# Kernel tuning notes

Hardware: AMD Instinct MI355X
Metric: run time of the kernel (lower is better)

## Reference

```python
import jax, jax.numpy as jnp
import numpy as np

EPS = 1e-5
NEG_INF = -1e38


def q_shift(x, H, W, gamma=0.25, s=1):
    # x: (B, T, C) with T = H*W. Four channel groups shifted by 1 pixel in +W,-W,+H,-H.
    B, T, C = x.shape
    g = int(C * gamma)
    x4 = x.reshape(B, H, W, C)
    o0 = jnp.pad(x4[..., 0:g], ((0, 0), (0, 0), (s, 0), (0, 0)))[:, :, :W, :]      # shift right along W
    o1 = jnp.pad(x4[..., g:2 * g], ((0, 0), (0, 0), (0, s), (0, 0)))[:, :, s:, :]  # shift left along W
    o2 = jnp.pad(x4[..., 2 * g:3 * g], ((0, 0), (s, 0), (0, 0), (0, 0)))[:, :H, :, :]  # shift down along H
    o3 = jnp.pad(x4[..., 3 * g:4 * g], ((0, 0), (0, s), (0, 0), (0, 0)))[:, s:, :, :]  # shift up along H
    parts = [o0, o1, o2, o3]
    if 4 * g < C:
        parts.append(jnp.zeros((B, H, W, C - 4 * g), x.dtype))
    return jnp.concatenate(parts, axis=-1).reshape(B, T, C)


def wkv(w, u, k, v):
    # Numerically-stable RWKV WKV recurrence.
    # w,u: (C,); k,v: (B,T,C) -> y: (B,T,C)
    B, T, C = k.shape

    def step(carry, kv):
        a, b, p = carry
        kt, vt = kv
        ww = u + kt
        p2 = jnp.maximum(p, ww)
        e1 = jnp.exp(p - p2)
        e2 = jnp.exp(ww - p2)
        y = (e1 * a + e2 * vt) / (e1 * b + e2)
        ww2 = p + w
        p3 = jnp.maximum(ww2, kt)
        f1 = jnp.exp(ww2 - p3)
        f2 = jnp.exp(kt - p3)
        return (f1 * a + f2 * vt, f1 * b + f2, p3), y

    init = (jnp.zeros((B, C), k.dtype), jnp.zeros((B, C), k.dtype),
            jnp.full((B, C), NEG_INF, k.dtype))
    kT = jnp.swapaxes(k, 0, 1)
    vT = jnp.swapaxes(v, 0, 1)
    _, ys = jax.lax.scan(step, init, (kT, vT))
    return jnp.swapaxes(ys, 0, 1)


def layer_norm(x, g, b):
    m = jnp.mean(x, axis=-1, keepdims=True)
    v = jnp.mean(jnp.square(x - m), axis=-1, keepdims=True)
    return (x - m) * jax.lax.rsqrt(v + EPS) * g + b


def setup_inputs() -> dict:
    key = jax.random.key(0)
    ks = jax.random.split(key, 16)
    B, H, W, C = 8, 64, 64, 768
    T = H * W
    sc = 1.0 / np.sqrt(C)
    inp = {
        "x": jax.random.normal(ks[0], (B, T, C), jnp.float32),
        "spatial_decay": jax.random.normal(ks[1], (C,), jnp.float32) * 0.1,
        "spatial_first": jax.random.normal(ks[2], (C,), jnp.float32) * 0.1,
        "mix_k": jax.random.uniform(ks[3], (1, 1, C), jnp.float32),
        "mix_v": jax.random.uniform(ks[4], (1, 1, C), jnp.float32),
        "mix_r": jax.random.uniform(ks[5], (1, 1, C), jnp.float32),
        "Wk": jax.random.normal(ks[6], (C, C), jnp.float32) * sc,
        "Wv": jax.random.normal(ks[7], (C, C), jnp.float32) * sc,
        "Wr": jax.random.normal(ks[8], (C, C), jnp.float32) * sc,
        "Wo": jax.random.normal(ks[9], (C, C), jnp.float32) * sc,
        "ln_g": jnp.ones((C,), jnp.float32),
        "ln_b": jnp.zeros((C,), jnp.float32),
        "Wd1": jax.random.normal(ks[10], (C, C // 4), jnp.float32) * sc,
        "bd1": jnp.zeros((C // 4,), jnp.float32),
        "Wd2": jax.random.normal(ks[11], (C // 4, C), jnp.float32) * (2.0 / np.sqrt(C)),
        "bd2": jnp.full((C,), -3.0, jnp.float32),
        "H": H,
        "W": W,
    }
    return inp


def reference(x, spatial_decay, spatial_first, mix_k, mix_v, mix_r,
              Wk, Wv, Wr, Wo, ln_g, ln_b, Wd1, bd1, Wd2, bd2, H, W):
    B, T, C = x.shape
    xx = q_shift(x, H, W)
    xk = x * mix_k + xx * (1.0 - mix_k)
    xv = x * mix_v + xx * (1.0 - mix_v)
    xr = x * mix_r + xx * (1.0 - mix_r)
    k = xk @ Wk
    v = xv @ Wv
    sr = jax.nn.sigmoid(xr @ Wr)
    # frequency-adaptive decay modulation from global context
    gctx = jnp.mean(x, axis=1)                       # (B, C)
    h = jnp.tanh(gctx @ Wd1 + bd1)                   # (B, C/4)
    mod = jax.nn.sigmoid(h @ Wd2 + bd2)              # (B, C)
    w = spatial_decay + jnp.mean(mod, axis=0)        # (C,)
    y = wkv(w, spatial_first, k, v)                  # (B, T, C)
    y = layer_norm(y, ln_g, ln_b)
    return (sr * y) @ Wo
```

## Files before the change

kernel.cpp:

```cpp
#include <hip/hip_runtime.h>
#include <hip/hip_bf16.h>

typedef __hip_bfloat16 bf16;
typedef short short8 __attribute__((ext_vector_type(8)));
typedef float f32x4 __attribute__((ext_vector_type(4)));

#define T_SEQ 4096
#define HH 64
#define WW2 64
#define C_DIM 768
#define CQ 192
#define LCH 32
#define NCH (T_SEQ / LCH)
#define NCG (C_DIM / 8)

__device__ __forceinline__ float b2f(bf16 h) { return __bfloat162float(h); }
__device__ __forceinline__ bf16 f2b(float f) { return __float2bfloat16(f); }
__device__ __forceinline__ float sigmoid_stable(float m) {
  float e = __expf(-fabsf(m));
  return (m >= 0.f) ? 1.f / (1.f + e) : e / (1.f + e);
}

union V16 { uint4 u; bf16 h[8]; };

__global__ void k_detect(const unsigned* __restrict__ p, int* __restrict__ flag) {
  if (threadIdx.x == 0 && blockIdx.x == 0)
    *flag = ((p[0] & 0xFFFFu) == 0u) ? 1 : 0;
}

__global__ void k_convert_b(const void* __restrict__ src, bf16* __restrict__ dst,
                            int n, const int* __restrict__ flag) {
  int i = blockIdx.x * blockDim.x + threadIdx.x;
  if (i >= n) return;
  dst[i] = (*flag) ? f2b(((const float*)src)[i]) : ((const bf16*)src)[i];
}

__global__ void k_convert_f(const void* __restrict__ src, float* __restrict__ dst,
                            int n, const int* __restrict__ flag) {
  int i = blockIdx.x * blockDim.x + threadIdx.x;
  if (i >= n) return;
  dst[i] = (*flag) ? ((const float*)src)[i] : b2f(((const bf16*)src)[i]);
}

__global__ void k_transpose_d(const void* __restrict__ src, bf16* __restrict__ dst,
                              const int* __restrict__ flag) {
  __shared__ bf16 tile[32][33];
  bool f32 = (*flag != 0);
  int bx = blockIdx.x * 32, by = blockIdx.y * 32;
  int tx = threadIdx.x, ty = threadIdx.y;
  for (int j = ty; j < 32; j += 8) {
    size_t idx = (size_t)(by + j) * C_DIM + bx + tx;
    tile[j][tx] = f32 ? f2b(((const float*)src)[idx]) : ((const bf16*)src)[idx];
  }
  __syncthreads();
  for (int j = ty; j < 32; j += 8)
    dst[(size_t)(bx + j) * C_DIM + by + tx] = tile[tx][j];
}

__global__ void k_shift_mix1(const void* __restrict__ xsrc,
                             const float* __restrict__ mix,
                             bf16* __restrict__ dst, int BT,
                             const int* __restrict__ flag) {
  int idx = blockIdx.x * blockDim.x + threadIdx.x;
  if (idx >= BT * (C_DIM / 8)) return;
  bool f32 = (*flag != 0);
  int c8 = (idx % (C_DIM / 8)) * 8;
  int tg = idx / (C_DIM / 8);
  int t = tg & (T_SEQ - 1);
  int hh = t >> 6, ww = t & (WW2 - 1);
  int g = c8 / CQ;
  int d; bool valid;
  if (g == 0)      { valid = (ww >= 1);        d = -1;   }
  else if (g == 1) { valid = (ww <= WW2 - 2);  d = 1;    }
  else if (g == 2) { valid = (hh >= 1);        d = -WW2; }
  else             { valid = (hh <= HH - 2);   d = WW2;  }
  ptrdiff_t base = (ptrdiff_t)tg * C_DIM + c8;
  float fx[8], fxx[8];
  if (f32) {
    const float* xp = (const float*)xsrc;
#pragma unroll
    for (int i = 0; i < 8; i++) fx[i] = xp[base + i];
    if (valid) {
#pragma unroll
      for (int i = 0; i < 8; i++) fxx[i] = xp[base + (ptrdiff_t)d * C_DIM + i];
    } else {
#pragma unroll
      for (int i = 0; i < 8; i++) fxx[i] = 0.f;
    }
  } else {
    const bf16* xp = (const bf16*)xsrc;
    V16 xin; xin.u = *(const uint4*)(xp + base);
    V16 xxv;
    if (valid) xxv.u = *(const uint4*)(xp + base + (ptrdiff_t)d * C_DIM);
    else       xxv.u = make_uint4(0u, 0u, 0u, 0u);
#pragma unroll
    for (int i = 0; i < 8; i++) { fx[i] = b2f(xin.h[i]); fxx[i] = b2f(xxv.h[i]); }
  }
  V16 o;
#pragma unroll
  for (int i = 0; i < 8; i++)
    o.h[i] = f2b(fxx[i] + mix[c8 + i] * (fx[i] - fxx[i]));
  *(uint4*)(dst + base) = o.u;
}

__global__ void k_gctx(const void* __restrict__ xsrc, float* __restrict__ gctx,
                       const int* __restrict__ flag) {
  bool f32 = (*flag != 0);
  int c = threadIdx.x;
  int chunk = blockIdx.x;
  int b = blockIdx.y;
  size_t base = ((size_t)b * T_SEQ + (size_t)chunk * 128) * C_DIM + c;
  float s = 0.f;
  if (f32) {
    const float* p = (const float*)xsrc;
    for (int t = 0; t < 128; t++) s += p[base + (size_t)t * C_DIM];
  } else {
    const bf16* p = (const bf16*)xsrc;
    for (int t = 0; t < 128; t++) s += b2f(p[base + (size_t)t * C_DIM]);
  }
  atomicAdd(&gctx[b * C_DIM + c], s);
}

__global__ void k_mod(const float* __restrict__ gctx,
                      const bf16* __restrict__ Wd1, const float* __restrict__ bd1,
                      const bf16* __restrict__ Wd2, const float* __restrict__ bd2,
                      float* __restrict__ wsum, int B) {
  __shared__ float hsh[CQ];
  int b = blockIdx.x, j = threadIdx.x;
  const float invT = 1.0f / (float)T_SEQ;
  float acc = bd1[j];
  for (int i = 0; i < C_DIM; i++)
    acc += (gctx[b * C_DIM + i] * invT) * b2f(Wd1[(size_t)i * CQ + j]);
  hsh[j] = tanhf(acc);
  __syncthreads();
  float invB = 1.0f / (float)B;
  for (int cc = j; cc < C_DIM; cc += CQ) {
    float m = bd2[cc];
    for (int jj = 0; jj < CQ; jj++)
      m += hsh[jj] * b2f(Wd2[(size_t)jj * C_DIM + cc]);
    atomicAdd(&wsum[cc], sigmoid_stable(m) * invB);
  }
}

__device__ __forceinline__ void g2l16(const void* g, void* s) {
  __builtin_amdgcn_global_load_lds(
      (const __attribute__((address_space(1))) unsigned int*)g,
      (__attribute__((address_space(3))) unsigned int*)s, 16, 0, 0);
}

template <int MODE>
__global__ __launch_bounds__(256) void k_gemm_bt(const bf16* __restrict__ A,
                                                 const bf16* __restrict__ Bt,
                                                 void* __restrict__ Cout,
                                                 const int* __restrict__ flag) {
  const int K = C_DIM, N = C_DIM;
  __shared__ bf16 sA[128 * 32];
  __shared__ bf16 sB[128 * 32];
  int tid = threadIdx.x;
  int wv = tid >> 6, lane = tid & 63;
  int lm = lane & 15, quad = lane >> 4;
  int m0 = blockIdx.x * 128, n0 = blockIdx.y * 128;
  int wm = (wv & 1) * 64, wn = (wv >> 1) * 64;
  bool f32out = (MODE == 2) && (*flag != 0);

  f32x4 acc[4][4];
#pragma unroll
  for (int i = 0; i < 4; i++)
#pragma unroll
    for (int j = 0; j < 4; j++) acc[i][j] = f32x4{0.f, 0.f, 0.f, 0.f};

  const bf16* Abase = A + (size_t)m0 * K;
  const bf16* Bbase = Bt + (size_t)n0 * K;
  int ci0 = wv * 128 + lane;
  int ci1 = wv * 128 + 64 + lane;

  for (int kc = 0; kc < K; kc += 32) {
    g2l16(Abase + (size_t)(ci0 >> 2) * K + kc + (ci0 & 3) * 8, (char*)sA + (size_t)(wv * 128) * 16);
    g2l16(Abase + (size_t)(ci1 >> 2) * K + kc + (ci1 & 3) * 8, (char*)sA + (size_t)(wv * 128 + 64) * 16);
    g2l16(Bbase + (size_t)(ci0 >> 2) * K + kc + (ci0 & 3) * 8, (char*)sB + (size_t)(wv * 128) * 16);
    g2l16(Bbase + (size_t)(ci1 >> 2) * K + kc + (ci1 & 3) * 8, (char*)sB + (size_t)(wv * 128 + 64) * 16);
    __syncthreads();
    short8 af[4], bfr[4];
#pragma unroll
    for (int i = 0; i < 4; i++)
      af[i] = *(const short8*)(sA + (size_t)(wm + i * 16 + lm) * 32 + quad * 8);
#pragma unroll
    for (int j = 0; j < 4; j++)
      bfr[j] = *(const short8*)(sB + (size_t)(wn + j * 16 + lm) * 32 + quad * 8);
#pragma unroll
    for (int i = 0; i < 4; i++)
#pragma unroll
      for (int j = 0; j < 4; j++)
        acc[i][j] = __builtin_amdgcn_mfma_f32_16x16x32_bf16(af[i], bfr[j], acc[i][j], 0, 0, 0);
    __syncthreads();
  }
#pragma unroll
  for (int i = 0; i < 4; i++)
#pragma unroll
    for (int j = 0; j < 4; j++)
#pragma unroll
      for (int r = 0; r < 4; r++) {
        int m = wm + i * 16 + quad * 4 + r;
        int n = wn + j * 16 + lm;
        float v = acc[i][j][r];
        if (MODE == 1) v = sigmoid_stable(v);
        size_t oidx = (size_t)(m0 + m) * N + n0 + n;
        if (MODE == 2) {
          if (f32out) ((float*)Cout)[oidx] = v;
          else        ((bf16*)Cout)[oidx] = f2b(v);
        } else {
          ((bf16*)Cout)[oidx] = f2b(v);
        }
      }
}


__global__ __launch_bounds__(256) void k_wkv_p1(
    const bf16* __restrict__ kb, const bf16* __restrict__ vb,
    const float* __restrict__ sd, const float* __restrict__ wsum,
    float* __restrict__ ca, float* __restrict__ cb, float* __restrict__ cp, int B) {
  int gid = blockIdx.x * 256 + threadIdx.x;
  if (gid >= B * NCH * NCG) return;
  int cg = gid % NCG;
  int ch = (gid / NCG) % NCH;
  int b  = gid / (NCG * NCH);
  int c0 = cg * 8;
  float w[8], a[8], bb[8], p[8];
#pragma unroll
  for (int i = 0; i < 8; i++) {
    w[i] = sd[c0 + i] + wsum[c0 + i];
    a[i] = 0.f; bb[i] = 0.f; p[i] = -1e38f;
  }
  const bf16* kp = kb + ((size_t)b * T_SEQ + (size_t)ch * LCH) * C_DIM + c0;
  const bf16* vp = vb + ((size_t)b * T_SEQ + (size_t)ch * LCH) * C_DIM + c0;
  V16 kv, vv, kn, vn;
  kv.u = *(const uint4*)kp;
  vv.u = *(const uint4*)vp;
  kn = kv; vn = vv;
  for (int t = 0; t < LCH; t++) {
    if (t + 1 < LCH) {
      kn.u = *(const uint4*)(kp + (size_t)(t + 1) * C_DIM);
      vn.u = *(const uint4*)(vp + (size_t)(t + 1) * C_DIM);
    }
#pragma unroll
    for (int i = 0; i < 8; i++) {
      float kt = b2f(kv.h[i]), vt = b2f(vv.h[i]);
      float ww2 = p[i] + w[i];
      float p3 = fmaxf(ww2, kt);
      float f1 = __expf(ww2 - p3);
      float f2 = __expf(kt - p3);
      a[i] = f1 * a[i] + f2 * vt;
      bb[i] = f1 * bb[i] + f2;
      p[i] = p3;
    }
    kv = kn; vv = vn;
  }
  size_t so = ((size_t)b * NCH + ch) * C_DIM + c0;
#pragma unroll
  for (int i = 0; i < 8; i++) { ca[so + i] = a[i]; cb[so + i] = bb[i]; cp[so + i] = p[i]; }
}

__global__ void k_wkv_p2(float* __restrict__ ca, float* __restrict__ cb,
                         float* __restrict__ cp,
                         const float* __restrict__ sd, const float* __restrict__ wsum,
                         int B) {
  int tid = blockIdx.x * blockDim.x + threadIdx.x;
  if (tid >= B * C_DIM) return;
  int b = tid / C_DIM, c = tid % C_DIM;
  float wL = (sd[c] + wsum[c]) * (float)LCH;
  float a = 0.f, bb = 0.f, p = -1e38f;
  for (int base = 0; base < NCH; base += 16) {
    float la[16], lb[16], lp[16];
#pragma unroll
    for (int j = 0; j < 16; j++) {
      size_t idx = ((size_t)b * NCH + base + j) * C_DIM + c;
      la[j] = ca[idx]; lb[j] = cb[idx]; lp[j] = cp[idx];
    }
#pragma unroll
    for (int j = 0; j < 16; j++) {
      size_t idx = ((size_t)b * NCH + base + j) * C_DIM + c;
      ca[idx] = a; cb[idx] = bb; cp[idx] = p;
      float pw = p + wL;
      float pn = fmaxf(pw, lp[j]);
      float e1 = __expf(pw - pn);
      float e2 = __expf(lp[j] - pn);
      a = e1 * a + e2 * la[j];
      bb = e1 * bb + e2 * lb[j];
      p = pn;
    }
  }
}

__global__ __launch_bounds__(256) void k_wkv_p3(
    const bf16* __restrict__ kb, const bf16* __restrict__ vb,
    const float* __restrict__ sd, const float* __restrict__ sf,
    const float* __restrict__ wsum,
    const float* __restrict__ ca, const float* __restrict__ cb,
    const float* __restrict__ cp, bf16* __restrict__ y, int B) {
  int gid = blockIdx.x * 256 + threadIdx.x;
  if (gid >= B * NCH * NCG) return;
  int cg = gid % NCG;
  int ch = (gid / NCG) % NCH;
  int b  = gid / (NCG * NCH);
  int c0 = cg * 8;
  size_t so = ((size_t)b * NCH + ch) * C_DIM + c0;
  float w[8], u[8], aa[8], bb[8], pp[8];
#pragma unroll
  for (int i = 0; i < 8; i++) {
    w[i] = sd[c0 + i] + wsum[c0 + i];
    u[i] = sf[c0 + i];
    aa[i] = ca[so + i]; bb[i] = cb[so + i]; pp[i] = cp[so + i];
  }
  const bf16* kp = kb + ((size_t)b * T_SEQ + (size_t)ch * LCH) * C_DIM + c0;
  const bf16* vp = vb + ((size_t)b * T_SEQ + (size_t)ch * LCH) * C_DIM + c0;
  bf16* yp = y + ((size_t)b * T_SEQ + (size_t)ch * LCH) * C_DIM + c0;
  V16 kv, vv, kn, vn;
  kv.u = *(const uint4*)kp;
  vv.u = *(const uint4*)vp;
  kn = kv; vn = vv;
  for (int t = 0; t < LCH; t++) {
    if (t + 1 < LCH) {
      kn.u = *(const uint4*)(kp + (size_t)(t + 1) * C_DIM);
      vn.u = *(const uint4*)(vp + (size_t)(t + 1) * C_DIM);
    }
    V16 o;
#pragma unroll
    for (int i = 0; i < 8; i++) {
      float kt = b2f(kv.h[i]), vt = b2f(vv.h[i]);
      float ww = u[i] + kt;
      float p2 = fmaxf(pp[i], ww);
      float e1 = __expf(pp[i] - p2);
      float e2 = __expf(ww - p2);
      o.h[i] = f2b((e1 * aa[i] + e2 * vt) / (e1 * bb[i] + e2));
      float ww2 = pp[i] + w[i];
      float p3 = fmaxf(ww2, kt);
      float f1 = __expf(ww2 - p3);
      float f2 = __expf(kt - p3);
      aa[i] = f1 * aa[i] + f2 * vt;
      bb[i] = f1 * bb[i] + f2;
      pp[i] = p3;
    }
    *(uint4*)(yp + (size_t)t * C_DIM) = o.u;
    kv = kn; vv = vn;
  }
}

__global__ __launch_bounds__(256) void k_ln_mul(const bf16* __restrict__ y,
                                                const bf16* __restrict__ sr,
                                                const float* __restrict__ lng,
                                                const float* __restrict__ lnb,
                                                bf16* __restrict__ out) {
  int row = blockIdx.x;
  int tid = threadIdx.x;
  const bf16* yr = y + (size_t)row * C_DIM;
  float v0 = b2f(yr[tid]), v1 = b2f(yr[tid + 256]), v2 = b2f(yr[tid + 512]);
  float s1 = v0 + v1 + v2;
  float s2 = v0 * v0 + v1 * v1 + v2 * v2;
#pragma unroll
  for (int off = 32; off >= 1; off >>= 1) {
    s1 += __shfl_xor(s1, off, 64);
    s2 += __shfl_xor(s2, off, 64);
  }
  __shared__ float sh1[4], sh2[4];
  int wv = tid >> 6, lane = tid & 63;
  if (lane == 0) { sh1[wv] = s1; sh2[wv] = s2; }
  __syncthreads();
  float t1 = sh1[0] + sh1[1] + sh1[2] + sh1[3];
  float t2 = sh2[0] + sh2[1] + sh2[2] + sh2[3];
  float mean = t1 * (1.f / (float)C_DIM);
  float var = t2 * (1.f / (float)C_DIM) - mean * mean;
  float rstd = rsqrtf(var + 1e-5f);
  const bf16* srr = sr + (size_t)row * C_DIM;
  bf16* orow = out + (size_t)row * C_DIM;
  float vv[3] = {v0, v1, v2};
#pragma unroll
  for (int kk = 0; kk < 3; kk++) {
    int c = tid + kk * 256;
    float r = (vv[kk] - mean) * rstd * lng[c] + lnb[c];
    orow[c] = f2b(r * b2f(srr[c]));
  }
}

extern "C" void kernel_launch(void* const* d_in, const int* in_sizes, int n_in,
                              void* d_out, int out_size, void* d_ws, size_t ws_size,
                              hipStream_t stream) {
  const void* x   = d_in[0];
  const void* sd  = d_in[1];
  const void* sf  = d_in[2];
  const void* mk  = d_in[3];
  const void* mv  = d_in[4];
  const void* mr  = d_in[5];
  const void* Wk  = d_in[6];
  const void* Wv  = d_in[7];
  const void* Wr  = d_in[8];
  const void* Wo  = d_in[9];
  const void* lng = d_in[10];
  const void* lnb = d_in[11];
  const void* Wd1 = d_in[12];
  const void* bd1 = d_in[13];
  const void* Wd2 = d_in[14];
  const void* bd2 = d_in[15];

  const int C = in_sizes[1];
  const int BT = in_sizes[0] / C;
  const int B = BT / T_SEQ;

  char* ws = (char*)d_ws;
  const size_t S = (size_t)BT * C * sizeof(bf16);
  const size_t WB = (size_t)C * C * sizeof(bf16);
  const size_t WD = (size_t)C * CQ * sizeof(bf16);
  bf16* slot0 = (bf16*)(ws + 0 * S);
  bf16* slot1 = (bf16*)(ws + 1 * S);
  char* p = ws + 2 * S;
  bf16* WkT = (bf16*)p; p += WB;
  bf16* WvT = (bf16*)p; p += WB;
  bf16* WrT = (bf16*)p; p += WB;
  bf16* WoT = (bf16*)p; p += WB;
  bf16* Wd1c = (bf16*)p; p += WD;
  bf16* Wd2c = (bf16*)p; p += WD;
  float* sd_f  = (float*)p; p += C * 4;
  float* sf_f  = (float*)p; p += C * 4;
  float* mk_f  = (float*)p; p += C * 4;
  float* mv_f  = (float*)p; p += C * 4;
  float* mr_f  = (float*)p; p += C * 4;
  float* lng_f = (float*)p; p += C * 4;
  float* lnb_f = (float*)p; p += C * 4;
  float* bd2_f = (float*)p; p += C * 4;
  float* bd1_f = (float*)p; p += CQ * 4;
  float* gctx  = (float*)p; p += (size_t)B * C * 4;
  float* wsum  = (float*)p; p += C * 4;
  int* flag    = (int*)p; p += 16;
  p = (char*)(((uintptr_t)p + 15) & ~(uintptr_t)15);
  float* ca = (float*)p; p += (size_t)B * NCH * C * 4;
  float* cb = (float*)p; p += (size_t)B * NCH * C * 4;
  float* cp = (float*)p; p += (size_t)B * NCH * C * 4;

  bf16* stage = (bf16*)d_out;

  k_detect<<<1, 64, 0, stream>>>((const unsigned*)lng, flag);
  hipMemsetAsync(gctx, 0, (size_t)(B * C + C) * sizeof(float), stream);

  k_convert_f<<<3, 256, 0, stream>>>(sd,  sd_f,  C, flag);
  k_convert_f<<<3, 256, 0, stream>>>(sf,  sf_f,  C, flag);
  k_convert_f<<<3, 256, 0, stream>>>(mk,  mk_f,  C, flag);
  k_convert_f<<<3, 256, 0, stream>>>(mv,  mv_f,  C, flag);
  k_convert_f<<<3, 256, 0, stream>>>(mr,  mr_f,  C, flag);
  k_convert_f<<<3, 256, 0, stream>>>(lng, lng_f, C, flag);
  k_convert_f<<<3, 256, 0, stream>>>(lnb, lnb_f, C, flag);
  k_convert_f<<<3, 256, 0, stream>>>(bd2, bd2_f, C, flag);
  k_convert_f<<<1, 256, 0, stream>>>(bd1, bd1_f, CQ, flag);
  k_convert_b<<<(C * CQ + 255) / 256, 256, 0, stream>>>(Wd1, Wd1c, C * CQ, flag);
  k_convert_b<<<(C * CQ + 255) / 256, 256, 0, stream>>>(Wd2, Wd2c, C * CQ, flag);

  dim3 tb(32, 8), tg(C / 32, C / 32);
  k_transpose_d<<<tg, tb, 0, stream>>>(Wk, WkT, flag);
  k_transpose_d<<<tg, tb, 0, stream>>>(Wv, WvT, flag);
  k_transpose_d<<<tg, tb, 0, stream>>>(Wr, WrT, flag);
  k_transpose_d<<<tg, tb, 0, stream>>>(Wo, WoT, flag);

  k_gctx<<<dim3(32, B), C, 0, stream>>>(x, gctx, flag);
  k_mod<<<B, CQ, 0, stream>>>(gctx, Wd1c, bd1_f, Wd2c, bd2_f, wsum, B);

  int nthr = BT * (C / 8);
  int nblk = (nthr + 255) / 256;
  dim3 gg(BT / 128, C / 128);

  k_shift_mix1<<<nblk, 256, 0, stream>>>(x, mk_f, stage, BT, flag);
  k_gemm_bt<0><<<gg, 256, 0, stream>>>(stage, WkT, slot0, flag);
  k_shift_mix1<<<nblk, 256, 0, stream>>>(x, mv_f, stage, BT, flag);
  k_gemm_bt<0><<<gg, 256, 0, stream>>>(stage, WvT, slot1, flag);

  int scan_threads = B * NCH * NCG;
  k_wkv_p1<<<(scan_threads + 255) / 256, 256, 0, stream>>>(slot0, slot1, sd_f, wsum, ca, cb, cp, B);
  k_wkv_p2<<<(B * C + 255) / 256, 256, 0, stream>>>(ca, cb, cp, sd_f, wsum, B);
  k_wkv_p3<<<(scan_threads + 255) / 256, 256, 0, stream>>>(slot0, slot1, sd_f, sf_f, wsum, ca, cb, cp, stage, B);

  k_shift_mix1<<<nblk, 256, 0, stream>>>(x, mr_f, slot0, BT, flag);
  k_gemm_bt<1><<<gg, 256, 0, stream>>>(slot0, WrT, slot1, flag);
  k_ln_mul<<<BT, 256, 0, stream>>>(stage, slot1, lng_f, lnb_f, slot0);
  k_gemm_bt<2><<<gg, 256, 0, stream>>>(slot0, WoT, d_out, flag);
}
```

Baseline: 716.2 us.

## Fuse prep kernels, merge k/v shift-mix, stage GEMM epilogue through LDS

Replaces the many tiny conversion/transpose launches and the flag-detect kernel with one prep kernel, one batched transpose kernel, and inline dtype detection. The k and v shift-mix passes are merged so x is read once for both. The GEMM epilogue now goes through shared memory so each row is written with wide vector stores, and the grid is reordered so N varies fastest. LayerNorm is vectorized with 192 threads handling 4 elements each. These target launch overhead, redundant reads of x, and scattered scalar stores, at the cost of extra LDS syncs in the epilogue.

```diff
diff --git a/kernel.cpp b/kernel.cpp
--- a/kernel.cpp
+++ b/kernel.cpp
@@ -20,32 +20,58 @@
   float e = __expf(-fabsf(m));
   return (m >= 0.f) ? 1.f / (1.f + e) : e / (1.f + e);
 }
+__device__ __forceinline__ bool is_f32(const void* lng) {
+  return ((const unsigned*)lng)[0] % 65536u == 0u;
+}
 
 union V16 { uint4 u; bf16 h[8]; };
-
-__global__ void k_detect(const unsigned* __restrict__ p, int* __restrict__ flag) {
-  if (threadIdx.x == 0 && blockIdx.x == 0)
-    *flag = ((p[0] & 0xFFFFu) == 0u) ? 1 : 0;
-}
-
-__global__ void k_convert_b(const void* __restrict__ src, bf16* __restrict__ dst,
-                            int n, const int* __restrict__ flag) {
-  int i = blockIdx.x * blockDim.x + threadIdx.x;
-  if (i >= n) return;
-  dst[i] = (*flag) ? f2b(((const float*)src)[i]) : ((const bf16*)src)[i];
-}
-
-__global__ void k_convert_f(const void* __restrict__ src, float* __restrict__ dst,
-                            int n, const int* __restrict__ flag) {
-  int i = blockIdx.x * blockDim.x + threadIdx.x;
-  if (i >= n) return;
-  dst[i] = (*flag) ? ((const float*)src)[i] : b2f(((const bf16*)src)[i]);
-}
-
-__global__ void k_transpose_d(const void* __restrict__ src, bf16* __restrict__ dst,
-                              const int* __restrict__ flag) {
+union V8f { float4 f; float x[4]; };
+
+__global__ void k_prep(const void* sd, const void* sf, const void* mk, const void* mv,
+                       const void* mr, const void* lng, const void* lnb, const void* bd2,
+                       const void* bd1, const void* Wd1, const void* Wd2,
+                       float* sd_f, float* sf_f, float* mk_f, float* mv_f, float* mr_f,
+                       float* lng_f, float* lnb_f, float* bd2_f, float* bd1_f,
+                       bf16* Wd1c, bf16* Wd2c) {
+  bool f32 = is_f32(lng);
+  int i = blockIdx.x * 256 + threadIdx.x;
+  if (i < 6144) {
+    int a = i / 768, idx = i % 768;
+    const void* s; float* d;
+    switch (a) {
+      case 0: s = sd;  d = sd_f;  break;
+      case 1: s = sf;  d = sf_f;  break;
+      case 2: s = mk;  d = mk_f;  break;
+      case 3: s = mv;  d = mv_f;  break;
+      case 4: s = mr;  d = mr_f;  break;
+      case 5: s = lng; d = lng_f; break;
+      case 6: s = lnb; d = lnb_f; break;
+      default: s = bd2; d = bd2_f; break;
+    }
+    d[idx] = f32 ? ((const float*)s)[idx] : b2f(((const bf16*)s)[idx]);
+  } else if (i < 6336) {
+    int idx = i - 6144;
+    bd1_f[idx] = f32 ? ((const float*)bd1)[idx] : b2f(((const bf16*)bd1)[idx]);
+  } else if (i < 6336 + 147456) {
+    int idx = i - 6336;
+    Wd1c[idx] = f32 ? f2b(((const float*)Wd1)[idx]) : ((const bf16*)Wd1)[idx];
+  } else if (i < 6336 + 294912) {
+    int idx = i - 153792;
+    Wd2c[idx] = f32 ? f2b(((const float*)Wd2)[idx]) : ((const bf16*)Wd2)[idx];
+  }
+}
+
+__global__ void k_transpose4(const void* W0, const void* W1, const void* W2, const void* W3,
+                             bf16* D0, bf16* D1, bf16* D2, bf16* D3, const void* lng) {
   __shared__ bf16 tile[32][33];
-  bool f32 = (*flag != 0);
+  bool f32 = is_f32(lng);
+  const void* src; bf16* dst;
+  switch (blockIdx.z) {
+    case 0: src = W0; dst = D0; break;
+    case 1: src = W1; dst = D1; break;
+    case 2: src = W2; dst = D2; break;
+    default: src = W3; dst = D3; break;
+  }
   int bx = blockIdx.x * 32, by = blockIdx.y * 32;
   int tx = threadIdx.x, ty = threadIdx.y;
   for (int j = ty; j < 32; j += 8) {
@@ -57,23 +83,27 @@
     dst[(size_t)(bx + j) * C_DIM + by + tx] = tile[tx][j];
 }
 
-__global__ void k_shift_mix1(const void* __restrict__ xsrc,
-                             const float* __restrict__ mix,
-                             bf16* __restrict__ dst, int BT,
-                             const int* __restrict__ flag) {
-  int idx = blockIdx.x * blockDim.x + threadIdx.x;
-  if (idx >= BT * (C_DIM / 8)) return;
-  bool f32 = (*flag != 0);
-  int c8 = (idx % (C_DIM / 8)) * 8;
-  int tg = idx / (C_DIM / 8);
-  int t = tg & (T_SEQ - 1);
+__device__ __forceinline__ void shift_geom(int t, int c8, int& d, bool& valid) {
   int hh = t >> 6, ww = t & (WW2 - 1);
   int g = c8 / CQ;
-  int d; bool valid;
   if (g == 0)      { valid = (ww >= 1);        d = -1;   }
   else if (g == 1) { valid = (ww <= WW2 - 2);  d = 1;    }
   else if (g == 2) { valid = (hh >= 1);        d = -WW2; }
   else             { valid = (hh <= HH - 2);   d = WW2;  }
+}
+
+__global__ void k_shift_mix2(const void* __restrict__ xsrc,
+                             const float* __restrict__ mka, const float* __restrict__ mva,
+                             bf16* __restrict__ dk, bf16* __restrict__ dv,
+                             int BT, const void* lng) {
+  int idx = blockIdx.x * blockDim.x + threadIdx.x;
+  if (idx >= BT * (C_DIM / 8)) return;
+  bool f32 = is_f32(lng);
+  int c8 = (idx % (C_DIM / 8)) * 8;
+  int tg = idx / (C_DIM / 8);
+  int t = tg & (T_SEQ - 1);
+  int d; bool valid;
+  shift_geom(t, c8, d, valid);
   ptrdiff_t base = (ptrdiff_t)tg * C_DIM + c8;
   float fx[8], fxx[8];
   if (f32) {
@@ -96,6 +126,50 @@
 #pragma unroll
     for (int i = 0; i < 8; i++) { fx[i] = b2f(xin.h[i]); fxx[i] = b2f(xxv.h[i]); }
   }
+  V16 ok, ov;
+#pragma unroll
+  for (int i = 0; i < 8; i++) {
+    float dd = fx[i] - fxx[i];
+    ok.h[i] = f2b(fxx[i] + mka[c8 + i] * dd);
+    ov.h[i] = f2b(fxx[i] + mva[c8 + i] * dd);
+  }
+  *(uint4*)(dk + base) = ok.u;
+  *(uint4*)(dv + base) = ov.u;
+}
+
+__global__ void k_shift_mix1(const void* __restrict__ xsrc,
+                             const float* __restrict__ mix,
+                             bf16* __restrict__ dst, int BT, const void* lng) {
+  int idx = blockIdx.x * blockDim.x + threadIdx.x;
+  if (idx >= BT * (C_DIM / 8)) return;
+  bool f32 = is_f32(lng);
+  int c8 = (idx % (C_DIM / 8)) * 8;
+  int tg = idx / (C_DIM / 8);
+  int t = tg & (T_SEQ - 1);
+  int d; bool valid;
+  shift_geom(t, c8, d, valid);
+  ptrdiff_t base = (ptrdiff_t)tg * C_DIM + c8;
+  float fx[8], fxx[8];
+  if (f32) {
+    const float* xp = (const float*)xsrc;
+#pragma unroll
+    for (int i = 0; i < 8; i++) fx[i] = xp[base + i];
+    if (valid) {
+#pragma unroll
+      for (int i = 0; i < 8; i++) fxx[i] = xp[base + (ptrdiff_t)d * C_DIM + i];
+    } else {
+#pragma unroll
+      for (int i = 0; i < 8; i++) fxx[i] = 0.f;
+    }
+  } else {
+    const bf16* xp = (const bf16*)xsrc;
+    V16 xin; xin.u = *(const uint4*)(xp + base);
+    V16 xxv;
+    if (valid) xxv.u = *(const uint4*)(xp + base + (ptrdiff_t)d * C_DIM);
+    else       xxv.u = make_uint4(0u, 0u, 0u, 0u);
+#pragma unroll
+    for (int i = 0; i < 8; i++) { fx[i] = b2f(xin.h[i]); fxx[i] = b2f(xxv.h[i]); }
+  }
   V16 o;
 #pragma unroll
   for (int i = 0; i < 8; i++)
@@ -104,8 +178,8 @@
 }
 
 __global__ void k_gctx(const void* __restrict__ xsrc, float* __restrict__ gctx,
-                       const int* __restrict__ flag) {
-  bool f32 = (*flag != 0);
+                       const void* lng) {
+  bool f32 = is_f32(lng);
   int c = threadIdx.x;
   int chunk = blockIdx.x;
   int b = blockIdx.y;
@@ -152,16 +226,18 @@
 __global__ __launch_bounds__(256) void k_gemm_bt(const bf16* __restrict__ A,
                                                  const bf16* __restrict__ Bt,
                                                  void* __restrict__ Cout,
-                                                 const int* __restrict__ flag) {
+                                                 const void* lng) {
   const int K = C_DIM, N = C_DIM;
-  __shared__ bf16 sA[128 * 32];
-  __shared__ bf16 sB[128 * 32];
+  __shared__ union {
+    struct { bf16 A[128 * 32]; bf16 B[128 * 32]; } kl;
+    float C[32 * 132];
+  } sh;
   int tid = threadIdx.x;
   int wv = tid >> 6, lane = tid & 63;
   int lm = lane & 15, quad = lane >> 4;
-  int m0 = blockIdx.x * 128, n0 = blockIdx.y * 128;
+  int m0 = blockIdx.y * 128, n0 = blockIdx.x * 128;
   int wm = (wv & 1) * 64, wn = (wv >> 1) * 64;
-  bool f32out = (MODE == 2) && (*flag != 0);
+  bool f32out = (MODE == 2) && is_f32(lng);
 
   f32x4 acc[4][4];
 #pragma unroll
@@ -175,18 +251,18 @@
   int ci1 = wv * 128 + 64 + lane;
 
   for (int kc = 0; kc < K; kc += 32) {
-    g2l16(Abase + (size_t)(ci0 >> 2) * K + kc + (ci0 & 3) * 8, (char*)sA + (size_t)(wv * 128) * 16);
-    g2l16(Abase + (size_t)(ci1 >> 2) * K + kc + (ci1 & 3) * 8, (char*)sA + (size_t)(wv * 128 + 64) * 16);
-    g2l16(Bbase + (size_t)(ci0 >> 2) * K + kc + (ci0 & 3) * 8, (char*)sB + (size_t)(wv * 128) * 16);
-    g2l16(Bbase + (size_t)(ci1 >> 2) * K + kc + (ci1 & 3) * 8, (char*)sB + (size_t)(wv * 128 + 64) * 16);
+    g2l16(Abase + (size_t)(ci0 >> 2) * K + kc + (ci0 & 3) * 8, (char*)sh.kl.A + (size_t)(wv * 128) * 16);
+    g2l16(Abase + (size_t)(ci1 >> 2) * K + kc + (ci1 & 3) * 8, (char*)sh.kl.A + (size_t)(wv * 128 + 64) * 16);
+    g2l16(Bbase + (size_t)(ci0 >> 2) * K + kc + (ci0 & 3) * 8, (char*)sh.kl.B + (size_t)(wv * 128) * 16);
+    g2l16(Bbase + (size_t)(ci1 >> 2) * K + kc + (ci1 & 3) * 8, (char*)sh.kl.B + (size_t)(wv * 128 + 64) * 16);
     __syncthreads();
     short8 af[4], bfr[4];
 #pragma unroll
     for (int i = 0; i < 4; i++)
-      af[i] = *(const short8*)(sA + (size_t)(wm + i * 16 + lm) * 32 + quad * 8);
+      af[i] = *(const short8*)(sh.kl.A + (size_t)(wm + i * 16 + lm) * 32 + quad * 8);
 #pragma unroll
     for (int j = 0; j < 4; j++)
-      bfr[j] = *(const short8*)(sB + (size_t)(wn + j * 16 + lm) * 32 + quad * 8);
+      bfr[j] = *(const short8*)(sh.kl.B + (size_t)(wn + j * 16 + lm) * 32 + quad * 8);
 #pragma unroll
     for (int i = 0; i < 4; i++)
 #pragma unroll
@@ -194,26 +270,44 @@
         acc[i][j] = __builtin_amdgcn_mfma_f32_16x16x32_bf16(af[i], bfr[j], acc[i][j], 0, 0, 0);
     __syncthreads();
   }
-#pragma unroll
-  for (int i = 0; i < 4; i++)
+
+  int rbase = (wm >> 2);
+  int row32 = tid >> 3, seg = tid & 7;
+  int gm_lo = m0 + ((row32 < 16) ? row32 : (64 + row32 - 16));
+#pragma unroll
+  for (int i = 0; i < 4; i++) {
+    if (i > 0) __syncthreads();
 #pragma unroll
     for (int j = 0; j < 4; j++)
 #pragma unroll
-      for (int r = 0; r < 4; r++) {
-        int m = wm + i * 16 + quad * 4 + r;
-        int n = wn + j * 16 + lm;
-        float v = acc[i][j][r];
-        if (MODE == 1) v = sigmoid_stable(v);
-        size_t oidx = (size_t)(m0 + m) * N + n0 + n;
-        if (MODE == 2) {
-          if (f32out) ((float*)Cout)[oidx] = v;
-          else        ((bf16*)Cout)[oidx] = f2b(v);
-        } else {
-          ((bf16*)Cout)[oidx] = f2b(v);
-        }
+      for (int r = 0; r < 4; r++)
+        sh.C[(rbase + quad * 4 + r) * 132 + wn + j * 16 + lm] = acc[i][j][r];
+    __syncthreads();
+    int gm = gm_lo + i * 16;
+    const float* src = &sh.C[row32 * 132 + seg * 16];
+    if (MODE == 2 && f32out) {
+      float* op = (float*)Cout + (size_t)gm * N + n0 + seg * 16;
+#pragma unroll
+      for (int q = 0; q < 4; q++) {
+        V8f t;
+#pragma unroll
+        for (int e = 0; e < 4; e++) t.x[e] = src[q * 4 + e];
+        *(float4*)(op + q * 4) = t.f;
       }
-}
-
+    } else {
+      V16 t0, t1;
+#pragma unroll
+      for (int e = 0; e < 8; e++) {
+        float v0 = src[e], v1 = src[8 + e];
+        if (MODE == 1) { v0 = sigmoid_stable(v0); v1 = sigmoid_stable(v1); }
+        t0.h[e] = f2b(v0); t1.h[e] = f2b(v1);
+      }
+      bf16* op = (bf16*)Cout + (size_t)gm * N + n0 + seg * 16;
+      *(uint4*)op = t0.u;
+      *(uint4*)(op + 8) = t1.u;
+    }
+  }
+}
 
 __global__ __launch_bounds__(256) void k_wkv_p1(
     const bf16* __restrict__ kb, const bf16* __restrict__ vb,
@@ -345,40 +439,50 @@
   }
 }
 
-__global__ __launch_bounds__(256) void k_ln_mul(const bf16* __restrict__ y,
+__global__ __launch_bounds__(192) void k_ln_mul(const bf16* __restrict__ y,
                                                 const bf16* __restrict__ sr,
                                                 const float* __restrict__ lng,
                                                 const float* __restrict__ lnb,
                                                 bf16* __restrict__ out) {
   int row = blockIdx.x;
   int tid = threadIdx.x;
+  int c0 = tid * 4;
   const bf16* yr = y + (size_t)row * C_DIM;
-  float v0 = b2f(yr[tid]), v1 = b2f(yr[tid + 256]), v2 = b2f(yr[tid + 512]);
-  float s1 = v0 + v1 + v2;
-  float s2 = v0 * v0 + v1 * v1 + v2 * v2;
+  union { uint2 u; bf16 h[4]; } yv;
+  yv.u = *(const uint2*)(yr + c0);
+  float v[4];
+  float s1 = 0.f, s2 = 0.f;
+#pragma unroll
+  for (int e = 0; e < 4; e++) {
+    v[e] = b2f(yv.h[e]);
+    s1 += v[e]; s2 += v[e] * v[e];
+  }
 #pragma unroll
   for (int off = 32; off >= 1; off >>= 1) {
     s1 += __shfl_xor(s1, off, 64);
     s2 += __shfl_xor(s2, off, 64);
   }
-  __shared__ float sh1[4], sh2[4];
+  __shared__ float sh1[3], sh2[3];
   int wv = tid >> 6, lane = tid & 63;
   if (lane == 0) { sh1[wv] = s1; sh2[wv] = s2; }
   __syncthreads();
-  float t1 = sh1[0] + sh1[1] + sh1[2] + sh1[3];
-  float t2 = sh2[0] + sh2[1] + sh2[2] + sh2[3];
+  float t1 = sh1[0] + sh1[1] + sh1[2];
+  float t2 = sh2[0] + sh2[1] + sh2[2];
   float mean = t1 * (1.f / (float)C_DIM);
   float var = t2 * (1.f / (float)C_DIM) - mean * mean;
   float rstd = rsqrtf(var + 1e-5f);
-  const bf16* srr = sr + (size_t)row * C_DIM;
-  bf16* orow = out + (size_t)row * C_DIM;
-  float vv[3] = {v0, v1, v2};
-#pragma unroll
-  for (int kk = 0; kk < 3; kk++) {
-    int c = tid + kk * 256;
-    float r = (vv[kk] - mean) * rstd * lng[c] + lnb[c];
-    orow[c] = f2b(r * b2f(srr[c]));
-  }
+  union { uint2 u; bf16 h[4]; } sv, ov;
+  sv.u = *(const uint2*)(sr + (size_t)row * C_DIM + c0);
+  float4 g = *(const float4*)(lng + c0);
+  float4 bvec = *(const float4*)(lnb + c0);
+  float gg[4] = {g.x, g.y, g.z, g.w};
+  float bb[4] = {bvec.x, bvec.y, bvec.z, bvec.w};
+#pragma unroll
+  for (int e = 0; e < 4; e++) {
+    float r = (v[e] - mean) * rstd * gg[e] + bb[e];
+    ov.h[e] = f2b(r * b2f(sv.h[e]));
+  }
+  *(uint2*)(out + (size_t)row * C_DIM + c0) = ov.u;
 }
 
 extern "C" void kernel_launch(void* const* d_in, const int* in_sizes, int n_in,
@@ -429,7 +533,6 @@
   float* bd1_f = (float*)p; p += CQ * 4;
   float* gctx  = (float*)p; p += (size_t)B * C * 4;
   float* wsum  = (float*)p; p += C * 4;
-  int* flag    = (int*)p; p += 16;
   p = (char*)(((uintptr_t)p + 15) & ~(uintptr_t)15);
   float* ca = (float*)p; p += (size_t)B * NCH * C * 4;
   float* cb = (float*)p; p += (size_t)B * NCH * C * 4;
@@ -437,46 +540,29 @@
 
   bf16* stage = (bf16*)d_out;
 
-  k_detect<<<1, 64, 0, stream>>>((const unsigned*)lng, flag);
   hipMemsetAsync(gctx, 0, (size_t)(B * C + C) * sizeof(float), stream);
 
-  k_convert_f<<<3, 256, 0, stream>>>(sd,  sd_f,  C, flag);
-  k_convert_f<<<3, 256, 0, stream>>>(sf,  sf_f,  C, flag);
-  k_convert_f<<<3, 256, 0, stream>>>(mk,  mk_f,  C, flag);
-  k_convert_f<<<3, 256, 0, stream>>>(mv,  mv_f,  C, flag);
-  k_convert_f<<<3, 256, 0, stream>>>(mr,  mr_f,  C, flag);
-  k_convert_f<<<3, 256, 0, stream>>>(lng, lng_f, C, flag);
-  k_convert_f<<<3, 256, 0, stream>>>(lnb, lnb_f, C, flag);
-  k_convert_f<<<3, 256, 0, stream>>>(bd2, bd2_f, C, flag);
-  k_convert_f<<<1, 256, 0, stream>>>(bd1, bd1_f, CQ, flag);
-  k_convert_b<<<(C * CQ + 255) / 256, 256, 0, stream>>>(Wd1, Wd1c, C * CQ, flag);
-  k_convert_b<<<(C * CQ + 255) / 256, 256, 0, stream>>>(Wd2, Wd2c, C * CQ, flag);
-
-  dim3 tb(32, 8), tg(C / 32, C / 32);
-  k_transpose_d<<<tg, tb, 0, stream>>>(Wk, WkT, flag);
-  k_transpose_d<<<tg, tb, 0, stream>>>(Wv, WvT, flag);
-  k_transpose_d<<<tg, tb, 0, stream>>>(Wr, WrT, flag);
-  k_transpose_d<<<tg, tb, 0, stream>>>(Wo, WoT, flag);
-
-  k_gctx<<<dim3(32, B), C, 0, stream>>>(x, gctx, flag);
+  k_prep<<<1177, 256, 0, stream>>>(sd, sf, mk, mv, mr, lng, lnb, bd2, bd1, Wd1, Wd2,
+                                   sd_f, sf_f, mk_f, mv_f, mr_f, lng_f, lnb_f, bd2_f,
+                                   bd1_f, Wd1c, Wd2c);
+  k_transpose4<<<dim3(24, 24, 4), dim3(32, 8), 0, stream>>>(Wk, Wv, Wr, Wo,
+                                                            WkT, WvT, WrT, WoT, lng);
+  k_gctx<<<dim3(32, B), C, 0, stream>>>(x, gctx, lng);
   k_mod<<<B, CQ, 0, stream>>>(gctx, Wd1c, bd1_f, Wd2c, bd2_f, wsum, B);
 
   int nthr = BT * (C / 8);
   int nblk = (nthr + 255) / 256;
-  dim3 gg(BT / 128, C / 128);
-
-  k_shift_mix1<<<nblk, 256, 0, stream>>>(x, mk_f, stage, BT, flag);
-  k_gemm_bt<0><<<gg, 256, 0, stream>>>(stage, WkT, slot0, flag);
-  k_shift_mix1<<<nblk, 256, 0, stream>>>(x, mv_f, stage, BT, flag);
-  k_gemm_bt<0><<<gg, 256, 0, stream>>>(stage, WvT, slot1, flag);
-
+  dim3 gg(C / 128, BT / 128);
+
+  k_shift_mix2<<<nblk, 256, 0, stream>>>(x, mk_f, mv_f, slot0, slot1, BT, lng);
+  k_gemm_bt<0><<<gg, 256, 0, stream>>>(slot0, WkT, stage, lng);
+  k_gemm_bt<0><<<gg, 256, 0, stream>>>(slot1, WvT, slot0, lng);
   int scan_threads = B * NCH * NCG;
-  k_wkv_p1<<<(scan_threads + 255) / 256, 256, 0, stream>>>(slot0, slot1, sd_f, wsum, ca, cb, cp, B);
+  k_wkv_p1<<<(scan_threads + 255) / 256, 256, 0, stream>>>(stage, slot0, sd_f, wsum, ca, cb, cp, B);
   k_wkv_p2<<<(B * C + 255) / 256, 256, 0, stream>>>(ca, cb, cp, sd_f, wsum, B);
-  k_wkv_p3<<<(scan_threads + 255) / 256, 256, 0, stream>>>(slot0, slot1, sd_f, sf_f, wsum, ca, cb, cp, stage, B);
-
-  k_shift_mix1<<<nblk, 256, 0, stream>>>(x, mr_f, slot0, BT, flag);
-  k_gemm_bt<1><<<gg, 256, 0, stream>>>(slot0, WrT, slot1, flag);
-  k_ln_mul<<<BT, 256, 0, stream>>>(stage, slot1, lng_f, lnb_f, slot0);
-  k_gemm_bt<2><<<gg, 256, 0, stream>>>(slot0, WoT, d_out, flag);
-}
+  k_wkv_p3<<<(scan_threads + 255) / 256, 256, 0, stream>>>(stage, slot0, sd_f, sf_f, wsum, ca, cb, cp, slot1, B);
+  k_shift_mix1<<<nblk, 256, 0, stream>>>(x, mr_f, slot0, BT, lng);
+  k_gemm_bt<1><<<gg, 256, 0, stream>>>(slot0, WrT, stage, lng);
+  k_ln_mul<<<BT, 192, 0, stream>>>(slot1, stage, lng_f, lnb_f, slot0);
+  k_gemm_bt<2><<<gg, 256, 0, stream>>>(slot0, WoT, d_out, lng);
+}
```

Measured after the change: 1.087 ms. 1.52x slower.
